# Optimization experiments

Measured on AMD Instinct MI355X. Metric: run time of the kernel, lower is better.

The kernel has to match this reference:

```python
import jax, jax.numpy as jnp
import numpy as np
from jax import lax

H, W = 320, 320
K = 21
P = (K - 1) // 2  # 10, replicate padding
LAM = 128.0
SIGMA_SPACE = 32.0
SIGMA_LUMA = 8.0
# all (i, j) kernel positions except the center -> 440 offsets
OFFSETS = np.array([(i, j) for i in range(K) for j in range(K)
                    if not (i == P and j == P)], dtype=np.int32)  # [440, 2]


def neighbor_diffs(x):
    """Shift-and-subtract equivalent of the sparse 21x21 conv.

    x: [H, W] -> [440, H, W] where out[k] = x - shift(x, offset_k)
    (replicate padding, matching Conv2d padding_mode='replicate' with a
    +1-at-center / -1-at-(i,j) kernel).
    """
    padded = jnp.pad(x, P, mode='edge')  # [H+2P, W+2P]

    def window(off):
        return lax.dynamic_slice(padded, (off[0], off[1]), (H, W))

    shifted = jax.vmap(window)(jnp.asarray(OFFSETS))  # [440, H, W]
    return x[None, :, :] - shifted


def setup_inputs() -> dict:
    key = jax.random.key(0)
    k_ref, k_tgt, k_noise = jax.random.split(key, 3)
    # random guidance image in [0, 255] like an RGB reference
    reference = jax.random.uniform(k_ref, (H, W, 3), dtype=jnp.float32) * 255.0
    target = jax.random.uniform(k_tgt, (H, W), dtype=jnp.float32)  # target/255
    # output parameter initialized at target (plus tiny noise so the data
    # term is non-degenerate)
    output = target + 0.01 * jax.random.normal(k_noise, (H, W), dtype=jnp.float32)

    # bilateral affinity weights w_ij, exactly as in __init__
    pos_x = jnp.broadcast_to(jnp.linspace(0.0, W, W)[None, :], (H, W))
    pos_y = jnp.broadcast_to(jnp.linspace(0.0, H, H)[:, None], (H, W))
    dpx = neighbor_diffs(pos_x)
    dpy = neighbor_diffs(pos_y)
    position_ij = -(dpx ** 2 + dpy ** 2) / (2.0 * SIGMA_SPACE ** 2)
    reference_ij = 0.0
    for c in range(3):
        reference_ij = reference_ij - neighbor_diffs(reference[:, :, c]) ** 2 / (2.0 * SIGMA_LUMA ** 2)
    w_ij = jnp.exp(position_ij + reference_ij)  # [440, H, W]

    return {"output": output, "target": target, "w_ij": w_ij}


def reference(output, target, w_ij):
    d = neighbor_diffs(output)  # [440, H, W]
    smooth = jnp.mean(w_ij * d * d)
    data = jnp.mean((output - target) ** 2)
    return H * W * LAM * smooth + data
```

## Files before the change

kernel.cpp:

```cpp
#include <hip/hip_runtime.h>
#include <cstddef>

constexpr int H_ = 320;
constexpr int W_ = 320;
constexpr int HW_ = H_ * W_;
constexpr int NK = 440;
constexpr int TS = 32;
constexpr int TPR = W_ / TS;
constexpr int NTILES = TPR * TPR;
constexpr int KC = 20;
constexpr int NKC = NK / KC;
constexpr int SMOOTH_BLOCKS = NTILES * NKC;
constexpr int NPART = SMOOTH_BLOCKS + NTILES;
constexpr int HALO = 10;
constexpr int LW = TS + 2 * HALO;
constexpr int LSTRIDE = LW + 1;

__device__ __forceinline__ int clampi(int v, int lo, int hi) {
    return v < lo ? lo : (v > hi ? hi : v);
}

__device__ __forceinline__ float block_reduce(float v, float* rbuf, int tid) {
    __syncthreads();
    for (int off = 32; off > 0; off >>= 1)
        v += __shfl_down(v, off, 64);
    if ((tid & 63) == 0) rbuf[tid >> 6] = v;
    __syncthreads();
    return rbuf[0] + rbuf[1] + rbuf[2] + rbuf[3];
}

__global__ __launch_bounds__(256) void bsl_main_kernel(
    const float* __restrict__ img,
    const float* __restrict__ tgt,
    const float* __restrict__ w,
    float* __restrict__ partials)
{
    __shared__ float lds[LW * LSTRIDE];
    __shared__ float rbuf[4];
    const int tid = threadIdx.x;

    const int tileId = blockIdx.x / NKC;
    const int kc     = blockIdx.x % NKC;
    const int ty = tileId / TPR, tx = tileId % TPR;
    const int y0 = ty * TS, x0 = tx * TS;

    for (int e = tid; e < LW * LW; e += 256) {
        const int ly = e / LW, lx = e - ly * LW;
        const int gy = clampi(y0 - HALO + ly, 0, H_ - 1);
        const int gx = clampi(x0 - HALO + lx, 0, W_ - 1);
        lds[ly * LSTRIDE + lx] = img[gy * W_ + gx];
    }
    __syncthreads();

    const int row = tid >> 3;
    const int c4  = (tid & 7) * 4;
    const int cbase = (HALO + row) * LSTRIDE + HALO + c4;
    const float c0 = lds[cbase + 0];
    const float c1 = lds[cbase + 1];
    const float c2 = lds[cbase + 2];
    const float c3 = lds[cbase + 3];

    float acc = 0.f;
    const float* wp = w + (size_t)(kc * KC) * HW_ + (y0 + row) * W_ + x0 + c4;
#pragma unroll 4
    for (int kk = 0; kk < KC; ++kk) {
        const int bk  = kc * KC + kk;
        const int idx = (bk < 220) ? bk : bk + 1;
        const int q   = idx / 21;
        const int di  = q - 10;
        const int dj  = idx - q * 21 - 10;

        const float4 w4 = *reinterpret_cast<const float4*>(wp);
        wp += HW_;

        const int nb = cbase + di * LSTRIDE + dj;
        const float n0 = lds[nb + 0];
        const float n1 = lds[nb + 1];
        const float n2 = lds[nb + 2];
        const float n3 = lds[nb + 3];
        const float d0 = c0 - n0, d1 = c1 - n1, d2 = c2 - n2, d3 = c3 - n3;
        acc += w4.x * d0 * d0;
        acc += w4.y * d1 * d1;
        acc += w4.z * d2 * d2;
        acc += w4.w * d3 * d3;
    }

    const float ssum = block_reduce(acc, rbuf, tid);
    if (tid == 0) partials[blockIdx.x] = ssum;

    if (kc == 0) {
        const float4 t4 = *reinterpret_cast<const float4*>(
            tgt + (y0 + row) * W_ + x0 + c4);
        const float d0 = c0 - t4.x, d1 = c1 - t4.y;
        const float d2 = c2 - t4.z, d3 = c3 - t4.w;
        const float dsum = block_reduce(d0*d0 + d1*d1 + d2*d2 + d3*d3, rbuf, tid);
        if (tid == 0) partials[SMOOTH_BLOCKS + tileId] = dsum;
    }
}

__global__ __launch_bounds__(256) void bsl_final_kernel(
    const float* __restrict__ partials, float* __restrict__ out)
{
    const int tid = threadIdx.x;
    double s = 0.0, d = 0.0;
    for (int i = tid; i < SMOOTH_BLOCKS; i += 256) s += (double)partials[i];
    for (int i = SMOOTH_BLOCKS + tid; i < NPART; i += 256) d += (double)partials[i];

    __shared__ double sm[256];
    __shared__ double sd[256];
    sm[tid] = s; sd[tid] = d;
    __syncthreads();
    for (int st = 128; st > 0; st >>= 1) {
        if (tid < st) { sm[tid] += sm[tid + st]; sd[tid] += sd[tid + st]; }
        __syncthreads();
    }
    if (tid == 0) {
        out[0] = (float)(128.0 * sm[0] / 440.0 + sd[0] / (double)HW_);
    }
}

extern "C" void kernel_launch(void* const* d_in, const int* in_sizes, int n_in,
                              void* d_out, int out_size, void* d_ws, size_t ws_size,
                              hipStream_t stream) {
    const float* img = (const float*)d_in[0];
    const float* tgt = (const float*)d_in[1];
    const float* wij = (const float*)d_in[2];
    float* out = (float*)d_out;
    float* partials = (float*)d_ws;

    bsl_main_kernel<<<SMOOTH_BLOCKS, 256, 0, stream>>>(img, tgt, wij, partials);
    bsl_final_kernel<<<1, 256, 0, stream>>>(partials, out);
}
```

Measured before the change: 37.88 us.

## Fuse final reduction via fixed-point atomics and last-block finalize; enlarge k-chunk

Replaces the separate final reduction kernel with 64-bit fixed-point atomic accumulation and a last-block-done counter, so only one kernel (plus a small memset) is launched. The k-chunk per block grows from 20 to 44, which means fewer blocks each reloading the LDS halo tile. The w_ij loads become nontemporal. The trade-offs are atomic contention, a fixed-point precision limit, and fewer blocks for the GPU to spread across its units.

```diff
diff --git a/kernel.cpp b/kernel.cpp
--- a/kernel.cpp
+++ b/kernel.cpp
@@ -8,13 +8,14 @@
 constexpr int TS = 32;
 constexpr int TPR = W_ / TS;
 constexpr int NTILES = TPR * TPR;
-constexpr int KC = 20;
+constexpr int KC = 44;
 constexpr int NKC = NK / KC;
 constexpr int SMOOTH_BLOCKS = NTILES * NKC;
-constexpr int NPART = SMOOTH_BLOCKS + NTILES;
 constexpr int HALO = 10;
 constexpr int LW = TS + 2 * HALO;
 constexpr int LSTRIDE = LW + 1;
+
+typedef float f32x4 __attribute__((ext_vector_type(4)));
 
 __device__ __forceinline__ int clampi(int v, int lo, int hi) {
     return v < lo ? lo : (v > hi ? hi : v);
@@ -29,11 +30,17 @@
     return rbuf[0] + rbuf[1] + rbuf[2] + rbuf[3];
 }
 
-__global__ __launch_bounds__(256) void bsl_main_kernel(
+__device__ __forceinline__ unsigned long long to_fx(float v) {
+    return (unsigned long long)(long long)((double)v * 4294967296.0);
+}
+
+__global__ __launch_bounds__(256) void bsl_fused_kernel(
     const float* __restrict__ img,
     const float* __restrict__ tgt,
     const float* __restrict__ w,
-    float* __restrict__ partials)
+    unsigned long long* __restrict__ acc,
+    unsigned int* __restrict__ counter,
+    float* __restrict__ out)
 {
     __shared__ float lds[LW * LSTRIDE];
     __shared__ float rbuf[4];
@@ -60,7 +67,7 @@
     const float c2 = lds[cbase + 2];
     const float c3 = lds[cbase + 3];
 
-    float acc = 0.f;
+    float sacc = 0.f;
     const float* wp = w + (size_t)(kc * KC) * HW_ + (y0 + row) * W_ + x0 + c4;
 #pragma unroll 4
     for (int kk = 0; kk < KC; ++kk) {
@@ -70,7 +77,7 @@
         const int di  = q - 10;
         const int dj  = idx - q * 21 - 10;
 
-        const float4 w4 = *reinterpret_cast<const float4*>(wp);
+        const f32x4 w4 = __builtin_nontemporal_load((const f32x4*)wp);
         wp += HW_;
 
         const int nb = cbase + di * LSTRIDE + dj;
@@ -79,43 +86,34 @@
         const float n2 = lds[nb + 2];
         const float n3 = lds[nb + 3];
         const float d0 = c0 - n0, d1 = c1 - n1, d2 = c2 - n2, d3 = c3 - n3;
-        acc += w4.x * d0 * d0;
-        acc += w4.y * d1 * d1;
-        acc += w4.z * d2 * d2;
-        acc += w4.w * d3 * d3;
+        sacc += w4.x * d0 * d0;
+        sacc += w4.y * d1 * d1;
+        sacc += w4.z * d2 * d2;
+        sacc += w4.w * d3 * d3;
     }
 
-    const float ssum = block_reduce(acc, rbuf, tid);
-    if (tid == 0) partials[blockIdx.x] = ssum;
+    const float ssum = block_reduce(sacc, rbuf, tid);
 
+    float dsum = 0.f;
     if (kc == 0) {
         const float4 t4 = *reinterpret_cast<const float4*>(
             tgt + (y0 + row) * W_ + x0 + c4);
         const float d0 = c0 - t4.x, d1 = c1 - t4.y;
         const float d2 = c2 - t4.z, d3 = c3 - t4.w;
-        const float dsum = block_reduce(d0*d0 + d1*d1 + d2*d2 + d3*d3, rbuf, tid);
-        if (tid == 0) partials[SMOOTH_BLOCKS + tileId] = dsum;
+        dsum = block_reduce(d0*d0 + d1*d1 + d2*d2 + d3*d3, rbuf, tid);
     }
-}
 
-__global__ __launch_bounds__(256) void bsl_final_kernel(
-    const float* __restrict__ partials, float* __restrict__ out)
-{
-    const int tid = threadIdx.x;
-    double s = 0.0, d = 0.0;
-    for (int i = tid; i < SMOOTH_BLOCKS; i += 256) s += (double)partials[i];
-    for (int i = SMOOTH_BLOCKS + tid; i < NPART; i += 256) d += (double)partials[i];
-
-    __shared__ double sm[256];
-    __shared__ double sd[256];
-    sm[tid] = s; sd[tid] = d;
-    __syncthreads();
-    for (int st = 128; st > 0; st >>= 1) {
-        if (tid < st) { sm[tid] += sm[tid + st]; sd[tid] += sd[tid + st]; }
-        __syncthreads();
-    }
     if (tid == 0) {
-        out[0] = (float)(128.0 * sm[0] / 440.0 + sd[0] / (double)HW_);
+        atomicAdd(&acc[0], to_fx(ssum));
+        if (kc == 0) atomicAdd(&acc[1], to_fx(dsum));
+        __threadfence();
+        const unsigned int old = atomicAdd(counter, 1u);
+        if (old == (unsigned int)(SMOOTH_BLOCKS - 1)) {
+            const long long a0 = (long long)atomicAdd(&acc[0], 0ull);
+            const long long a1 = (long long)atomicAdd(&acc[1], 0ull);
+            out[0] = (float)(128.0 * (double)a0 / (4294967296.0 * 440.0)
+                             + (double)a1 / (4294967296.0 * 102400.0));
+        }
     }
 }
 
@@ -126,8 +124,9 @@
     const float* tgt = (const float*)d_in[1];
     const float* wij = (const float*)d_in[2];
     float* out = (float*)d_out;
-    float* partials = (float*)d_ws;
+    unsigned long long* acc = (unsigned long long*)d_ws;
+    unsigned int* counter = (unsigned int*)((char*)d_ws + 16);
 
-    bsl_main_kernel<<<SMOOTH_BLOCKS, 256, 0, stream>>>(img, tgt, wij, partials);
-    bsl_final_kernel<<<1, 256, 0, stream>>>(partials, out);
+    hipMemsetAsync(d_ws, 0, 24, stream);
+    bsl_fused_kernel<<<SMOOTH_BLOCKS, 256, 0, stream>>>(img, tgt, wij, acc, counter, out);
 }
```

Result: slower. 84.23 us (+122.3%).

## Tile by full-width row strips with multiple quads per thread and nontemporal weight loads

Applied to the files above, without the earlier changes.

Replaces 32x32 tiles with 16-row full-width strips, so each block loads a wide halo once and each thread handles five float4 quads per offset. Weight reads become fully contiguous 5 KB row spans and use nontemporal loads, since w_ij is streamed once. The offset chunk size drops to 11 and the unroll is removed, giving 800 blocks with more work each. This lowers the per-element halo overhead and improves memory coalescing. The cost is more registers and larger LDS per block, which may reduce occupancy.

```diff
diff --git a/kernel.cpp b/kernel.cpp
--- a/kernel.cpp
+++ b/kernel.cpp
@@ -5,16 +5,19 @@
 constexpr int W_ = 320;
 constexpr int HW_ = H_ * W_;
 constexpr int NK = 440;
-constexpr int TS = 32;
-constexpr int TPR = W_ / TS;
-constexpr int NTILES = TPR * TPR;
-constexpr int KC = 20;
+constexpr int SR = 16;
+constexpr int NSTRIP = H_ / SR;
+constexpr int KC = 11;
 constexpr int NKC = NK / KC;
-constexpr int SMOOTH_BLOCKS = NTILES * NKC;
-constexpr int NPART = SMOOTH_BLOCKS + NTILES;
+constexpr int SMOOTH_BLOCKS = NSTRIP * NKC;
+constexpr int NPART = SMOOTH_BLOCKS + NSTRIP;
 constexpr int HALO = 10;
-constexpr int LW = TS + 2 * HALO;
-constexpr int LSTRIDE = LW + 1;
+constexpr int LROWS = SR + 2 * HALO;
+constexpr int LCOLS = W_ + 2 * HALO;
+constexpr int LSTRIDE = LCOLS + 1;
+constexpr int NQ = SR * W_ / (256 * 4);
+
+typedef float f32x4 __attribute__((ext_vector_type(4)));
 
 __device__ __forceinline__ int clampi(int v, int lo, int hi) {
     return v < lo ? lo : (v > hi ? hi : v);
@@ -35,66 +38,82 @@
     const float* __restrict__ w,
     float* __restrict__ partials)
 {
-    __shared__ float lds[LW * LSTRIDE];
+    __shared__ float lds[LROWS * LSTRIDE];
     __shared__ float rbuf[4];
     const int tid = threadIdx.x;
 
-    const int tileId = blockIdx.x / NKC;
-    const int kc     = blockIdx.x % NKC;
-    const int ty = tileId / TPR, tx = tileId % TPR;
-    const int y0 = ty * TS, x0 = tx * TS;
+    const int strip = blockIdx.x / NKC;
+    const int kc    = blockIdx.x % NKC;
+    const int y0 = strip * SR;
 
-    for (int e = tid; e < LW * LW; e += 256) {
-        const int ly = e / LW, lx = e - ly * LW;
+    for (int e = tid; e < LROWS * LCOLS; e += 256) {
+        const int ly = e / LCOLS, lx = e - ly * LCOLS;
         const int gy = clampi(y0 - HALO + ly, 0, H_ - 1);
-        const int gx = clampi(x0 - HALO + lx, 0, W_ - 1);
+        const int gx = clampi(lx - HALO, 0, W_ - 1);
         lds[ly * LSTRIDE + lx] = img[gy * W_ + gx];
     }
     __syncthreads();
 
-    const int row = tid >> 3;
-    const int c4  = (tid & 7) * 4;
-    const int cbase = (HALO + row) * LSTRIDE + HALO + c4;
-    const float c0 = lds[cbase + 0];
-    const float c1 = lds[cbase + 1];
-    const float c2 = lds[cbase + 2];
-    const float c3 = lds[cbase + 3];
+    int   cbase[NQ];
+    float c[NQ][4];
+#pragma unroll
+    for (int i = 0; i < NQ; ++i) {
+        const int p  = i * 1024 + tid * 4;
+        const int r  = p / W_;
+        const int cc = p - r * W_;
+        cbase[i] = (HALO + r) * LSTRIDE + HALO + cc;
+        c[i][0] = lds[cbase[i] + 0];
+        c[i][1] = lds[cbase[i] + 1];
+        c[i][2] = lds[cbase[i] + 2];
+        c[i][3] = lds[cbase[i] + 3];
+    }
 
-    float acc = 0.f;
-    const float* wp = w + (size_t)(kc * KC) * HW_ + (y0 + row) * W_ + x0 + c4;
-#pragma unroll 4
+    float sacc = 0.f;
+    const float* wp = w + (size_t)(kc * KC) * HW_ + y0 * W_ + tid * 4;
+#pragma unroll 1
     for (int kk = 0; kk < KC; ++kk) {
         const int bk  = kc * KC + kk;
         const int idx = (bk < 220) ? bk : bk + 1;
         const int q   = idx / 21;
-        const int di  = q - 10;
-        const int dj  = idx - q * 21 - 10;
+        const int soff = (q - 10) * LSTRIDE + (idx - q * 21 - 10);
 
-        const float4 w4 = *reinterpret_cast<const float4*>(wp);
+        f32x4 wv[NQ];
+#pragma unroll
+        for (int i = 0; i < NQ; ++i)
+            wv[i] = __builtin_nontemporal_load((const f32x4*)(wp + i * 1024));
+
+#pragma unroll
+        for (int i = 0; i < NQ; ++i) {
+            const int nb = cbase[i] + soff;
+            const float n0 = lds[nb + 0];
+            const float n1 = lds[nb + 1];
+            const float n2 = lds[nb + 2];
+            const float n3 = lds[nb + 3];
+            const float d0 = c[i][0] - n0, d1 = c[i][1] - n1;
+            const float d2 = c[i][2] - n2, d3 = c[i][3] - n3;
+            sacc += wv[i].x * d0 * d0;
+            sacc += wv[i].y * d1 * d1;
+            sacc += wv[i].z * d2 * d2;
+            sacc += wv[i].w * d3 * d3;
+        }
         wp += HW_;
-
-        const int nb = cbase + di * LSTRIDE + dj;
-        const float n0 = lds[nb + 0];
-        const float n1 = lds[nb + 1];
-        const float n2 = lds[nb + 2];
-        const float n3 = lds[nb + 3];
-        const float d0 = c0 - n0, d1 = c1 - n1, d2 = c2 - n2, d3 = c3 - n3;
-        acc += w4.x * d0 * d0;
-        acc += w4.y * d1 * d1;
-        acc += w4.z * d2 * d2;
-        acc += w4.w * d3 * d3;
     }
 
-    const float ssum = block_reduce(acc, rbuf, tid);
+    const float ssum = block_reduce(sacc, rbuf, tid);
     if (tid == 0) partials[blockIdx.x] = ssum;
 
     if (kc == 0) {
-        const float4 t4 = *reinterpret_cast<const float4*>(
-            tgt + (y0 + row) * W_ + x0 + c4);
-        const float d0 = c0 - t4.x, d1 = c1 - t4.y;
-        const float d2 = c2 - t4.z, d3 = c3 - t4.w;
-        const float dsum = block_reduce(d0*d0 + d1*d1 + d2*d2 + d3*d3, rbuf, tid);
-        if (tid == 0) partials[SMOOTH_BLOCKS + tileId] = dsum;
+        float dacc = 0.f;
+        const float* tp = tgt + y0 * W_ + tid * 4;
+#pragma unroll
+        for (int i = 0; i < NQ; ++i) {
+            const float4 t4 = *reinterpret_cast<const float4*>(tp + i * 1024);
+            const float d0 = c[i][0] - t4.x, d1 = c[i][1] - t4.y;
+            const float d2 = c[i][2] - t4.z, d3 = c[i][3] - t4.w;
+            dacc += d0 * d0 + d1 * d1 + d2 * d2 + d3 * d3;
+        }
+        const float dsum = block_reduce(dacc, rbuf, tid);
+        if (tid == 0) partials[SMOOTH_BLOCKS + strip] = dsum;
     }
 }
 
@@ -104,7 +123,7 @@
     const int tid = threadIdx.x;
     double s = 0.0, d = 0.0;
     for (int i = tid; i < SMOOTH_BLOCKS; i += 256) s += (double)partials[i];
-    for (int i = SMOOTH_BLOCKS + tid; i < NPART; i += 256) d += (double)partials[i];
+    if (tid < NSTRIP) d = (double)partials[SMOOTH_BLOCKS + tid];
 
     __shared__ double sm[256];
     __shared__ double sd[256];
```

After: 44.30 us. +16.9%, slower.
